# Kernel optimization log

Measured on AMD Instinct MI355X. Metric: run time of the kernel, lower is better.

Reference implementation:

```python
import jax, jax.numpy as jnp
import numpy as np

WINDOW = 256  # sw_attention_window_size; query i attends to keys j with i-WINDOW <= j <= i


def setup_inputs() -> dict:
    key = jax.random.key(0)
    kq, kk, kv = jax.random.split(key, 3)
    shape = (4, 16, 4096, 64)  # [B, H, S, D]
    q = jax.random.normal(kq, shape, dtype=jnp.float32)
    k = jax.random.normal(kk, shape, dtype=jnp.float32)
    v = jax.random.normal(kv, shape, dtype=jnp.float32)
    return {"q": q, "k": k, "v": v}


def _local_attention(q, k, v, window):
    # Block-banded sliding-window attention: mask (j >= i - window) & (j <= i).
    # Uses block size == window so each query block only needs 2 key blocks.
    b, h, S, d = q.shape
    W = window
    T = S // W  # number of query blocks
    scale = jnp.asarray(d, q.dtype) ** -0.5  # flex_attention default scale

    qb = q.reshape(b, h, T, W, d)  # [b,h,T,W,d]

    def windows(x):
        # pad one block of zeros in front, then each query block t sees
        # key positions [t*W - W, t*W + W) == blocks (t, t+1) of the padded seq
        xp = jnp.pad(x, ((0, 0), (0, 0), (W, 0), (0, 0)))
        blk = xp.reshape(b, h, T + 1, W, d)
        return jnp.concatenate([blk[:, :, :-1], blk[:, :, 1:]], axis=3)  # [b,h,T,2W,d]

    kw = windows(k)
    vw = windows(v)

    # mask: global i = t*W + qi, global j = t*W - W + kj
    qi = jnp.arange(W)[:, None]          # [W,1]
    kj = jnp.arange(2 * W)[None, :]      # [1,2W]
    band = (kj >= qi) & (kj <= qi + W)   # i-W <= j <= i   -> [W,2W]
    t = jnp.arange(T)[:, None, None]     # [T,1,1]
    valid = (t * W - W + kj[None, :, :]) >= 0  # j >= 0 (drop padded keys)
    mask = band[None, :, :] & valid      # [T,W,2W]

    scores = jnp.einsum('bhtqd,bhtkd->bhtqk', qb, kw) * scale  # [b,h,T,W,2W]
    scores = jnp.where(mask[None, None], scores, -jnp.inf)
    attn = jax.nn.softmax(scores, axis=-1)
    out = jnp.einsum('bhtqk,bhtkd->bhtqd', attn, vw)
    return out.reshape(b, h, S, d)


def reference(q, k, v):
    return _local_attention(q, k, v, WINDOW)
```

## Files before the change

kernel.cpp:

```cpp
#include <hip/hip_runtime.h>

typedef __attribute__((ext_vector_type(8))) short bf16x8;
typedef __attribute__((ext_vector_type(4))) float f32x4;

#define L2E 1.44269504088896340736f

__device__ __forceinline__ unsigned pk2(float lo, float hi) {
    unsigned r;
    asm("v_cvt_pk_bf16_f32 %0, %1, %2" : "=v"(r) : "v"(lo), "v"(hi));
    return r;
}

constexpr int D_   = 64;
constexpr int SEQ  = 4096;
constexpr int MQ   = 128;
constexpr int CK   = 128;
constexpr int KSTR = 72;
constexpr int VSTR = 132;
constexpr int OSTR = 68;

constexpr int SMEM_BYTES = 35840;

__global__ __launch_bounds__(256, 2)
void swattn_kernel(const float* __restrict__ Qg, const float* __restrict__ Kg,
                   const float* __restrict__ Vg, float* __restrict__ Og)
{
    __shared__ __align__(16) char smem[SMEM_BYTES];
    unsigned short* k_lds = (unsigned short*)smem;
    unsigned short* v_lds = (unsigned short*)(smem + CK * KSTR * 2);
    float*          o_lds = (float*)smem;

    const int tid  = threadIdx.x;
    const int wv   = tid >> 6;
    const int lane = tid & 63;
    const int g    = lane >> 4;
    const int n    = lane & 15;

    const int bh = blockIdx.x & 63;
    const int qb = blockIdx.x >> 6;
    const size_t base = (size_t)bh * SEQ * D_;
    const int q0 = qb * MQ;

    bf16x8 qf[2][2];
    #pragma unroll
    for (int nt = 0; nt < 2; ++nt) {
        const float* qp = Qg + base + (size_t)(q0 + wv * 32 + nt * 16 + n) * D_;
        #pragma unroll
        for (int ks = 0; ks < 2; ++ks) {
            f32x4 a = *(const f32x4*)(qp + ks * 32 + g * 8);
            f32x4 b = *(const f32x4*)(qp + ks * 32 + g * 8 + 4);
            union { bf16x8 v; unsigned u[4]; } t;
            t.u[0] = pk2(a.x * 0.125f, a.y * 0.125f);
            t.u[1] = pk2(a.z * 0.125f, a.w * 0.125f);
            t.u[2] = pk2(b.x * 0.125f, b.y * 0.125f);
            t.u[3] = pk2(b.z * 0.125f, b.w * 0.125f);
            qf[nt][ks] = t.v;
        }
    }

    f32x4 o_ac[4][2];
    #pragma unroll
    for (int a = 0; a < 4; ++a)
        #pragma unroll
        for (int b = 0; b < 2; ++b)
            o_ac[a][b] = f32x4{0.f, 0.f, 0.f, 0.f};
    float m_r[2] = {-1e30f, -1e30f};
    float l_r[2] = {0.0f, 0.0f};

    #pragma unroll
    for (int ci = 0; ci < 3; ++ci) {
        const int cb = qb - 2 + ci;
        if (cb < 0) continue;

        __syncthreads();

        {
            const f32x4* kp = (const f32x4*)(Kg + base + (size_t)cb * CK * D_);
            #pragma unroll
            for (int i = 0; i < 8; ++i) {
                int idx = tid + 256 * i;
                int row = idx >> 4, c4 = idx & 15;
                f32x4 x = kp[idx];
                *(uint2*)&k_lds[row * KSTR + c4 * 4] =
                    make_uint2(pk2(x.x, x.y), pk2(x.z, x.w));
            }
        }
        {
            const f32x4* vp = (const f32x4*)(Vg + base + (size_t)cb * CK * D_);
            const int g16 = tid & 15, kq = tid >> 4;
            #pragma unroll
            for (int h = 0; h < 2; ++h) {
                int key0 = (kq + 16 * h) * 4;
                union { f32x4 v; float f[4]; } r0, r1, r2, r3;
                r0.v = vp[(key0 + 0) * 16 + g16];
                r1.v = vp[(key0 + 1) * 16 + g16];
                r2.v = vp[(key0 + 2) * 16 + g16];
                r3.v = vp[(key0 + 3) * 16 + g16];
                #pragma unroll
                for (int i = 0; i < 4; ++i) {
                    *(uint2*)&v_lds[(g16 * 4 + i) * VSTR + key0] =
                        make_uint2(pk2(r0.f[i], r1.f[i]), pk2(r2.f[i], r3.f[i]));
                }
            }
        }
        __syncthreads();

        f32x4 sc[8][2];
        #pragma unroll
        for (int mt = 0; mt < 8; ++mt)
            #pragma unroll
            for (int nt = 0; nt < 2; ++nt)
                sc[mt][nt] = f32x4{0.f, 0.f, 0.f, 0.f};

        __builtin_amdgcn_s_setprio(1);
        #pragma unroll
        for (int ks = 0; ks < 2; ++ks) {
            #pragma unroll
            for (int mt = 0; mt < 8; ++mt) {
                bf16x8 af = *(const bf16x8*)&k_lds[(mt * 16 + n) * KSTR + ks * 32 + g * 8];
                sc[mt][0] = __builtin_amdgcn_mfma_f32_16x16x32_bf16(af, qf[0][ks], sc[mt][0], 0, 0, 0);
                sc[mt][1] = __builtin_amdgcn_mfma_f32_16x16x32_bf16(af, qf[1][ks], sc[mt][1], 0, 0, 0);
            }
        }
        __builtin_amdgcn_s_setprio(0);

        if (ci != 1) {
            #pragma unroll
            for (int mt = 0; mt < 8; ++mt)
                #pragma unroll
                for (int nt = 0; nt < 2; ++nt)
                    #pragma unroll
                    for (int r = 0; r < 4; ++r) {
                        int kk = mt * 16 + g * 4 + r;
                        int qq = wv * 32 + nt * 16 + n;
                        bool ok = (ci == 0) ? (kk >= qq) : (kk <= qq);
                        if (!ok) sc[mt][nt][r] = -1e30f;
                    }
        }

        uint2 pkv[8][2];
        #pragma unroll
        for (int nt = 0; nt < 2; ++nt) {
            float t8[8];
            #pragma unroll
            for (int mt = 0; mt < 8; ++mt)
                t8[mt] = fmaxf(fmaxf(sc[mt][nt][0], sc[mt][nt][1]),
                               fmaxf(sc[mt][nt][2], sc[mt][nt][3]));
            float ma = fmaxf(t8[0], t8[1]), mb = fmaxf(t8[2], t8[3]);
            float mc = fmaxf(t8[4], t8[5]), md = fmaxf(t8[6], t8[7]);
            float mx = fmaxf(fmaxf(ma, mb), fmaxf(mc, md));
            mx = fmaxf(mx, __shfl_xor(mx, 16, 64));
            mx = fmaxf(mx, __shfl_xor(mx, 32, 64));
            float mnew = fmaxf(m_r[nt], mx);
            float al   = __builtin_amdgcn_exp2f((m_r[nt] - mnew) * L2E);
            m_r[nt] = mnew;
            float c  = -mnew * L2E;
            float s8[8];
            #pragma unroll
            for (int mt = 0; mt < 8; ++mt) {
                float p0 = __builtin_amdgcn_exp2f(fmaf(sc[mt][nt][0], L2E, c));
                float p1 = __builtin_amdgcn_exp2f(fmaf(sc[mt][nt][1], L2E, c));
                float p2 = __builtin_amdgcn_exp2f(fmaf(sc[mt][nt][2], L2E, c));
                float p3 = __builtin_amdgcn_exp2f(fmaf(sc[mt][nt][3], L2E, c));
                s8[mt] = (p0 + p1) + (p2 + p3);
                pkv[mt][nt] = make_uint2(pk2(p0, p1), pk2(p2, p3));
            }
            float ra = s8[0] + s8[1], rb = s8[2] + s8[3];
            float rc = s8[4] + s8[5], rd = s8[6] + s8[7];
            float rs = (ra + rb) + (rc + rd);
            rs += __shfl_xor(rs, 16, 64);
            rs += __shfl_xor(rs, 32, 64);
            l_r[nt] = l_r[nt] * al + rs;
            #pragma unroll
            for (int mtd = 0; mtd < 4; ++mtd)
                #pragma unroll
                for (int r = 0; r < 4; ++r)
                    o_ac[mtd][nt][r] *= al;
        }

        __builtin_amdgcn_s_setprio(1);
        #pragma unroll
        for (int kp4 = 0; kp4 < 4; ++kp4) {
            bf16x8 bfr[2];
            #pragma unroll
            for (int nt = 0; nt < 2; ++nt) {
                union { bf16x8 v; uint2 u2[2]; } bb;
                bb.u2[0] = pkv[2 * kp4][nt];
                bb.u2[1] = pkv[2 * kp4 + 1][nt];
                bfr[nt] = bb.v;
            }
            #pragma unroll
            for (int mtd = 0; mtd < 4; ++mtd) {
                int bus = (mtd * 16 + n) * VSTR + kp4 * 32 + g * 4;
                union { bf16x8 v; uint2 u2[2]; } aa;
                aa.u2[0] = *(const uint2*)&v_lds[bus];
                aa.u2[1] = *(const uint2*)&v_lds[bus + 16];
                o_ac[mtd][0] = __builtin_amdgcn_mfma_f32_16x16x32_bf16(aa.v, bfr[0], o_ac[mtd][0], 0, 0, 0);
                o_ac[mtd][1] = __builtin_amdgcn_mfma_f32_16x16x32_bf16(aa.v, bfr[1], o_ac[mtd][1], 0, 0, 0);
            }
        }
        __builtin_amdgcn_s_setprio(0);
    }

    __syncthreads();
    float inv[2] = {1.0f / l_r[0], 1.0f / l_r[1]};
    #pragma unroll
    for (int mtd = 0; mtd < 4; ++mtd)
        #pragma unroll
        for (int nt = 0; nt < 2; ++nt) {
            f32x4 v = o_ac[mtd][nt];
            v.x *= inv[nt]; v.y *= inv[nt]; v.z *= inv[nt]; v.w *= inv[nt];
            *(f32x4*)&o_lds[(wv * 32 + nt * 16 + n) * OSTR + mtd * 16 + g * 4] = v;
        }
    __syncthreads();

    f32x4* op = (f32x4*)(Og + base + (size_t)q0 * D_);
    #pragma unroll
    for (int p = 0; p < 8; ++p) {
        int row = p * 16 + (tid >> 4);
        int c4  = tid & 15;
        f32x4 v = *(const f32x4*)&o_lds[row * OSTR + c4 * 4];
        op[row * 16 + c4] = v;
    }
}

extern "C" void kernel_launch(void* const* d_in, const int* in_sizes, int n_in,
                              void* d_out, int out_size, void* d_ws, size_t ws_size,
                              hipStream_t stream) {
    (void)in_sizes; (void)n_in; (void)out_size; (void)d_ws; (void)ws_size;
    const float* q = (const float*)d_in[0];
    const float* k = (const float*)d_in[1];
    const float* v = (const float*)d_in[2];
    float* o = (float*)d_out;
    dim3 grid(64 * 32), block(256);
    hipLaunchKernelGGL(swattn_kernel, grid, block, 0, stream, q, k, v, o);
}
```

Before: 230.2 us.

## Prefetch next K/V chunk into registers while computing current chunk

Register-level software pipelining of the K/V chunk loads. The next chunk's global loads are issued right after the current chunk is written to LDS, so their latency overlaps the QK and PV MFMA work. The loop is no longer unrolled and now runs over a variable chunk count. This adds 16 f32x4 registers per thread, which may pressure occupancy under launch_bounds(256,2), and the mask direction becomes a runtime branch instead of a compile-time one.

```diff
diff --git a/kernel.cpp b/kernel.cpp
--- a/kernel.cpp
+++ b/kernel.cpp
@@ -40,6 +40,8 @@
     const int qb = blockIdx.x >> 6;
     const size_t base = (size_t)bh * SEQ * D_;
     const int q0 = qb * MQ;
+
+    const int g16 = tid & 15, kq = tid >> 4;
 
     bf16x8 qf[2][2];
     #pragma unroll
@@ -67,40 +69,62 @@
     float m_r[2] = {-1e30f, -1e30f};
     float l_r[2] = {0.0f, 0.0f};
 
-    #pragma unroll
-    for (int ci = 0; ci < 3; ++ci) {
-        const int cb = qb - 2 + ci;
-        if (cb < 0) continue;
+    const int cb0 = (qb >= 2) ? (qb - 2) : 0;
+    const int nc  = (qb >= 2) ? 3 : (qb + 1);
+
+    f32x4 kr[8], vr[8];
+    {
+        const f32x4* kp = (const f32x4*)(Kg + base + (size_t)cb0 * CK * D_);
+        const f32x4* vp = (const f32x4*)(Vg + base + (size_t)cb0 * CK * D_);
+        #pragma unroll
+        for (int i = 0; i < 8; ++i) kr[i] = kp[tid + 256 * i];
+        #pragma unroll
+        for (int h = 0; h < 2; ++h) {
+            int key0 = (kq + 16 * h) * 4;
+            #pragma unroll
+            for (int r = 0; r < 4; ++r)
+                vr[h * 4 + r] = vp[(key0 + r) * 16 + g16];
+        }
+    }
+
+    for (int t = 0; t < nc; ++t) {
+        const int cb = cb0 + t;
+        const int ci = cb - qb + 2;
 
         __syncthreads();
 
-        {
-            const f32x4* kp = (const f32x4*)(Kg + base + (size_t)cb * CK * D_);
-            #pragma unroll
-            for (int i = 0; i < 8; ++i) {
-                int idx = tid + 256 * i;
-                int row = idx >> 4, c4 = idx & 15;
-                f32x4 x = kp[idx];
-                *(uint2*)&k_lds[row * KSTR + c4 * 4] =
-                    make_uint2(pk2(x.x, x.y), pk2(x.z, x.w));
-            }
-        }
-        {
-            const f32x4* vp = (const f32x4*)(Vg + base + (size_t)cb * CK * D_);
-            const int g16 = tid & 15, kq = tid >> 4;
+        #pragma unroll
+        for (int i = 0; i < 8; ++i) {
+            int idx = tid + 256 * i;
+            int row = idx >> 4, c4 = idx & 15;
+            f32x4 x = kr[i];
+            *(uint2*)&k_lds[row * KSTR + c4 * 4] =
+                make_uint2(pk2(x.x, x.y), pk2(x.z, x.w));
+        }
+        #pragma unroll
+        for (int h = 0; h < 2; ++h) {
+            int key0 = (kq + 16 * h) * 4;
+            union { f32x4 v; float f[4]; } r0, r1, r2, r3;
+            r0.v = vr[h * 4 + 0]; r1.v = vr[h * 4 + 1];
+            r2.v = vr[h * 4 + 2]; r3.v = vr[h * 4 + 3];
+            #pragma unroll
+            for (int i = 0; i < 4; ++i) {
+                *(uint2*)&v_lds[(g16 * 4 + i) * VSTR + key0] =
+                    make_uint2(pk2(r0.f[i], r1.f[i]), pk2(r2.f[i], r3.f[i]));
+            }
+        }
+
+        if (t + 1 < nc) {
+            const f32x4* kp = (const f32x4*)(Kg + base + (size_t)(cb + 1) * CK * D_);
+            const f32x4* vp = (const f32x4*)(Vg + base + (size_t)(cb + 1) * CK * D_);
+            #pragma unroll
+            for (int i = 0; i < 8; ++i) kr[i] = kp[tid + 256 * i];
             #pragma unroll
             for (int h = 0; h < 2; ++h) {
                 int key0 = (kq + 16 * h) * 4;
-                union { f32x4 v; float f[4]; } r0, r1, r2, r3;
-                r0.v = vp[(key0 + 0) * 16 + g16];
-                r1.v = vp[(key0 + 1) * 16 + g16];
-                r2.v = vp[(key0 + 2) * 16 + g16];
-                r3.v = vp[(key0 + 3) * 16 + g16];
                 #pragma unroll
-                for (int i = 0; i < 4; ++i) {
-                    *(uint2*)&v_lds[(g16 * 4 + i) * VSTR + key0] =
-                        make_uint2(pk2(r0.f[i], r1.f[i]), pk2(r2.f[i], r3.f[i]));
-                }
+                for (int r = 0; r < 4; ++r)
+                    vr[h * 4 + r] = vp[(key0 + r) * 16 + g16];
             }
         }
         __syncthreads();
@@ -125,6 +149,7 @@
         __builtin_amdgcn_s_setprio(0);
 
         if (ci != 1) {
+            const bool lower = (ci == 0);
             #pragma unroll
             for (int mt = 0; mt < 8; ++mt)
                 #pragma unroll
@@ -133,7 +158,7 @@
                     for (int r = 0; r < 4; ++r) {
                         int kk = mt * 16 + g * 4 + r;
                         int qq = wv * 32 + nt * 16 + n;
-                        bool ok = (ci == 0) ? (kk >= qq) : (kk <= qq);
+                        bool ok = lower ? (kk >= qq) : (kk <= qq);
                         if (!ok) sc[mt][nt][r] = -1e30f;
                     }
         }
```

New measurement: 248.5 us. 1.08x slower.
